# Performance work log

Hardware: AMD Instinct MI355X
Metric: run time of the kernel (lower is better)

## Reference

```python
import jax, jax.numpy as jnp
import numpy as np

EPS = 1e-9
NUM_HEADS = 16
D = 1024      # input_dim == hidden_dim
B, S = 2, 2048


def layer_norm(x, scale, shift):
    mu = x.mean(axis=-1, keepdims=True)
    # torch std is unbiased (ddof=1); eps added to std, not variance
    std = jnp.std(x, axis=-1, ddof=1, keepdims=True)
    return scale * (x - mu) / (std + EPS) + shift


def setup_inputs() -> dict:
    key = jax.random.key(0)
    ks = jax.random.split(key, 18)
    d, h = D, D
    w = lambda k, sh: jax.random.normal(k, sh, dtype=jnp.float32) * 0.02
    return {
        "inputs": jax.random.normal(ks[0], (B, S, d), dtype=jnp.float32),
        "ln1_scale": jax.random.normal(ks[1], (d,), dtype=jnp.float32),
        "ln1_shift": jax.random.normal(ks[2], (d,), dtype=jnp.float32),
        "Wq": w(ks[3], (d, h)), "bq": jnp.zeros((h,), jnp.float32),
        "Wk": w(ks[4], (d, h)), "bk": jnp.zeros((h,), jnp.float32),
        "Wv": w(ks[5], (d, h)), "bv": jnp.zeros((h,), jnp.float32),
        "Wo": w(ks[6], (h, d)), "bo": jnp.zeros((d,), jnp.float32),
        "W1": w(ks[7], (d, 4 * d)), "b1": jnp.zeros((4 * d,), jnp.float32),
        "W2": w(ks[8], (4 * d, d)), "b2": jnp.zeros((d,), jnp.float32),
        "ln2_scale": jax.random.normal(ks[9], (d,), dtype=jnp.float32),
        "ln2_shift": jax.random.normal(ks[10], (d,), dtype=jnp.float32),
    }


def mhsa(x, Wq, bq, Wk, bk, Wv, bv, Wo, bo):
    b, s, d = x.shape
    nh, dh = NUM_HEADS, D // NUM_HEADS
    q = (x @ Wq + bq).reshape(b, s, nh, dh).transpose(0, 2, 1, 3)  # b h s d
    k = (x @ Wk + bk).reshape(b, s, nh, dh).transpose(0, 2, 1, 3)
    v = (x @ Wv + bv).reshape(b, s, nh, dh).transpose(0, 2, 1, 3)
    scores = jnp.einsum("bhqd,bhkd->bhqk", q, k) / jnp.sqrt(jnp.float32(dh))
    causal = jnp.triu(jnp.ones((s, s), dtype=bool), k=1)  # mask above diagonal
    scores = jnp.where(causal, -jnp.inf, scores)
    p = jax.nn.softmax(scores, axis=-1)
    p = jnp.where(jnp.isnan(p), 0.0, p)  # NaN-fill as in original
    out = jnp.einsum("bhqk,bhkd->bhqd", p, v)
    out = out.transpose(0, 2, 1, 3).reshape(b, s, nh * dh)
    return out @ Wo + bo


def reference(inputs, ln1_scale, ln1_shift, Wq, bq, Wk, bk, Wv, bv, Wo, bo,
              W1, b1, W2, b2, ln2_scale, ln2_shift):
    o1 = layer_norm(inputs, ln1_scale, ln1_shift)
    o1 = mhsa(o1, Wq, bq, Wk, bk, Wv, bv, Wo, bo) + inputs
    o2 = layer_norm(o1, ln2_scale, ln2_shift)
    # NOTE: original adds the residual from the *normalized* tensor, not o1
    ffn = jax.nn.relu(o2 @ W1 + b1) @ W2 + b2
    return ffn + o2
```

## Files before the change

kernel.cpp:

```cpp
#include <hip/hip_runtime.h>
#include <hip/hip_bf16.h>
#include <math.h>

#define BB 2
#define SS 2048
#define DD 1024
#define HH 16
#define DH 64
#define NROW (BB*SS)
#define FFN (4*DD)

typedef __attribute__((ext_vector_type(8))) __bf16 bf16x8;
typedef __attribute__((ext_vector_type(4))) __bf16 bf16x4;
typedef __attribute__((ext_vector_type(4))) float f32x4;

#define QSCALE 0.18033688011112042f

__device__ __forceinline__ ushort f2b(float f) {
    union { float f; uint32_t u; } x; x.f = f;
    uint32_t r = x.u + 0x7FFF + ((x.u >> 16) & 1);
    return (ushort)(r >> 16);
}
__device__ __forceinline__ float b2f(ushort u) {
    union { uint32_t u; float f; } x; x.u = (uint32_t)u << 16;
    return x.f;
}

__global__ __launch_bounds__(256)
void ln_kernel(const float* __restrict__ x, const float* __restrict__ scale,
               const float* __restrict__ shift, ushort* __restrict__ y) {
    int row = blockIdx.x;
    const float* xr = x + (size_t)row * DD;
    ushort* yr = y + (size_t)row * DD;
    int t = threadIdx.x;
    float v[4];
    float s = 0.f, ss = 0.f;
#pragma unroll
    for (int i = 0; i < 4; ++i) {
        v[i] = xr[t + 256 * i];
        s += v[i];
        ss += v[i] * v[i];
    }
#pragma unroll
    for (int off = 32; off; off >>= 1) {
        s  += __shfl_xor(s, off);
        ss += __shfl_xor(ss, off);
    }
    __shared__ float red[8];
    int w = t >> 6;
    if ((t & 63) == 0) { red[w] = s; red[w + 4] = ss; }
    __syncthreads();
    float st  = red[0] + red[1] + red[2] + red[3];
    float sst = red[4] + red[5] + red[6] + red[7];
    float mu = st * (1.f / DD);
    float var = (sst - DD * mu * mu) * (1.f / (DD - 1));
    var = fmaxf(var, 0.f);
    float inv = 1.f / (sqrtf(var) + 1e-9f);
#pragma unroll
    for (int i = 0; i < 4; ++i) {
        int c = t + 256 * i;
        yr[c] = f2b(scale[c] * (v[i] - mu) * inv + shift[c]);
    }
}

__global__ __launch_bounds__(256)
void ln_res4_kernel(const ushort* __restrict__ p, const float* __restrict__ pbias,
                    const float* __restrict__ xb,
                    const float* __restrict__ scale, const float* __restrict__ shift,
                    ushort* __restrict__ yb) {
    const size_t MN = (size_t)NROW * DD;
    int row = blockIdx.x;
    ushort* ybr = yb + (size_t)row * DD;
    int t = threadIdx.x;
    float v[4];
    float s = 0.f, ss = 0.f;
#pragma unroll
    for (int i = 0; i < 4; ++i) {
        int c = t + 256 * i;
        size_t idx = (size_t)row * DD + c;
        float sum = b2f(p[idx]) + b2f(p[MN + idx]) + b2f(p[2 * MN + idx])
                  + b2f(p[3 * MN + idx]) + pbias[c] + xb[idx];
        v[i] = sum;
        s += sum;
        ss += sum * sum;
    }
#pragma unroll
    for (int off = 32; off; off >>= 1) {
        s  += __shfl_xor(s, off);
        ss += __shfl_xor(ss, off);
    }
    __shared__ float red[8];
    int w = t >> 6;
    if ((t & 63) == 0) { red[w] = s; red[w + 4] = ss; }
    __syncthreads();
    float st  = red[0] + red[1] + red[2] + red[3];
    float sst = red[4] + red[5] + red[6] + red[7];
    float mu = st * (1.f / DD);
    float var = (sst - DD * mu * mu) * (1.f / (DD - 1));
    var = fmaxf(var, 0.f);
    float inv = 1.f / (sqrtf(var) + 1e-9f);
#pragma unroll
    for (int i = 0; i < 4; ++i) {
        int c = t + 256 * i;
        ybr[c] = f2b(scale[c] * (v[i] - mu) * inv + shift[c]);
    }
}

__global__ __launch_bounds__(256)
void transpose_bf16_kernel(const float* __restrict__ W, ushort* __restrict__ Wt,
                           int K, int N) {
    __shared__ ushort tile[32][33];
    int tx = threadIdx.x & 31;
    int ty = threadIdx.x >> 5;
    int n0 = blockIdx.x * 32;
    int k0 = blockIdx.y * 32;
#pragma unroll
    for (int i = 0; i < 32; i += 8)
        tile[ty + i][tx] = f2b(W[(size_t)(k0 + ty + i) * N + n0 + tx]);
    __syncthreads();
#pragma unroll
    for (int i = 0; i < 32; i += 8)
        Wt[(size_t)(n0 + ty + i) * K + k0 + tx] = tile[tx][ty + i];
}

__global__ __launch_bounds__(256)
void transpose4_bf16_kernel(const float* __restrict__ W0, const float* __restrict__ W1,
                            const float* __restrict__ W2, const float* __restrict__ W3,
                            ushort* __restrict__ Wt) {
    __shared__ ushort tile[32][33];
    int z = blockIdx.z;
    const float* W = z == 0 ? W0 : (z == 1 ? W1 : (z == 2 ? W2 : W3));
    ushort* dst = Wt + (size_t)z * DD * DD;
    int tx = threadIdx.x & 31;
    int ty = threadIdx.x >> 5;
    int n0 = blockIdx.x * 32;
    int k0 = blockIdx.y * 32;
#pragma unroll
    for (int i = 0; i < 32; i += 8)
        tile[ty + i][tx] = f2b(W[(size_t)(k0 + ty + i) * DD + n0 + tx]);
    __syncthreads();
#pragma unroll
    for (int i = 0; i < 32; i += 8)
        dst[(size_t)(n0 + ty + i) * DD + k0 + tx] = tile[tx][ty + i];
}

__global__ __launch_bounds__(256)
void reduce_ffn2_kernel(const ushort* __restrict__ p, const float* __restrict__ bias,
                        const ushort* __restrict__ res, float* __restrict__ out) {
    const size_t MN = (size_t)NROW * DD;
    int i = (blockIdx.x * 256 + threadIdx.x) * 4;
    ushort4 a = *reinterpret_cast<const ushort4*>(p + i);
    ushort4 b = *reinterpret_cast<const ushort4*>(p + MN + i);
    ushort4 c4 = *reinterpret_cast<const ushort4*>(p + 2 * MN + i);
    ushort4 d4 = *reinterpret_cast<const ushort4*>(p + 3 * MN + i);
    ushort4 r = *reinterpret_cast<const ushort4*>(res + i);
    int c = i & (DD - 1);
    float4 bs = *reinterpret_cast<const float4*>(bias + c);
    float4 o;
    o.x = b2f(a.x) + b2f(b.x) + b2f(c4.x) + b2f(d4.x) + bs.x + b2f(r.x);
    o.y = b2f(a.y) + b2f(b.y) + b2f(c4.y) + b2f(d4.y) + bs.y + b2f(r.y);
    o.z = b2f(a.z) + b2f(b.z) + b2f(c4.z) + b2f(d4.z) + bs.z + b2f(r.z);
    o.w = b2f(a.w) + b2f(b.w) + b2f(c4.w) + b2f(d4.w) + bs.w + b2f(r.w);
    *reinterpret_cast<float4*>(out + i) = o;
}

#define GBM 128
#define GBK 32

template <int MODE, bool BF16_OUT, int DEPTH, int BN>
__global__ __launch_bounds__(512)
void gemm_bf16_kernel(const ushort* __restrict__ A, const ushort* __restrict__ Wt,
                      const float* __restrict__ bias, const ushort* __restrict__ addsrc,
                      void* __restrict__ Cout, int M, int N, int K, int lda,
                      const float* __restrict__ bias2, const float* __restrict__ bias3,
                      void* __restrict__ out2, void* __restrict__ out3) {
    __shared__ ushort As[DEPTH][GBM * GBK];
    __shared__ ushort Bs[DEPTH][BN * GBK];
    constexpr int NF = BN / 64;

    int tid = threadIdx.x;
    int lane = tid & 63;
    int wid = tid >> 6;
    int wr = wid >> 2, wc = wid & 3;

    int gx = gridDim.x;
    int nwg = gx * gridDim.y;
    int orig = blockIdx.y * gx + blockIdx.x;
    int q8 = nwg >> 3;
    int swz = (orig & 7) * q8 + (orig >> 3);
    int bx = swz % gx, by = swz / gx;

    int brow = by * GBM;
    int bcol = bx * BN;
    size_t koff = (size_t)blockIdx.z * K;

    int lrow = lane & 15;
    int kgrp = lane >> 4;

    f32x4 acc[4][NF] = {};

    auto stage = [&](int buf, int k0) {
        {
            int row = tid >> 2;
            int gran = (tid & 3) ^ ((row >> 1) & 3);
            const char* ga = (const char*)A +
                ((size_t)(brow + row) * lda + koff + k0) * 2 + gran * 16;
            __builtin_amdgcn_global_load_lds(
                (const __attribute__((address_space(1))) uint32_t*)ga,
                (__attribute__((address_space(3))) uint32_t*)(&As[buf][0] + (wid * 16) * GBK),
                16, 0, 0);
        }
#pragma unroll
        for (int i = 0; i < BN / 128; ++i) {
            int idx = i * 512 + tid;
            int row = idx >> 2;
            int gran = (idx & 3) ^ ((row >> 1) & 3);
            const char* gb = (const char*)Wt +
                ((size_t)(bcol + row) * lda + koff + k0) * 2 + gran * 16;
            __builtin_amdgcn_global_load_lds(
                (const __attribute__((address_space(1))) uint32_t*)gb,
                (__attribute__((address_space(3))) uint32_t*)(&Bs[buf][0] + (i * 128 + wid * 16) * GBK),
                16, 0, 0);
        }
    };

    int nk = K / GBK;
    constexpr int PRE = DEPTH - 1;
#pragma unroll
    for (int s = 0; s < PRE; ++s)
        if (s < nk) stage(s, s * GBK);

    int cur = 0, stg = PRE;
    for (int t = 0; t < nk; ++t) {
        __builtin_amdgcn_sched_barrier(0);
        int rem = nk - 1 - t;
        if constexpr (DEPTH == 3 && BN == 128) {
            if (rem >= 1)      asm volatile("s_waitcnt vmcnt(2)" ::: "memory");
            else               asm volatile("s_waitcnt vmcnt(0)" ::: "memory");
        } else if constexpr (DEPTH == 3 && BN == 256) {
            if (rem >= 1)      asm volatile("s_waitcnt vmcnt(3)" ::: "memory");
            else               asm volatile("s_waitcnt vmcnt(0)" ::: "memory");
        } else {
            asm volatile("s_waitcnt vmcnt(0)" ::: "memory");
        }
        asm volatile("s_barrier" ::: "memory");
        if (t + PRE < nk) stage(stg, (t + PRE) * GBK);

        bf16x8 afrag[4], bfrag[NF];
#pragma unroll
        for (int mi = 0; mi < 4; ++mi) {
            int row = wr * 64 + mi * 16 + lrow;
            int gran = kgrp ^ ((row >> 1) & 3);
            afrag[mi] = *(const bf16x8*)((const char*)&As[cur][0] + row * 64 + gran * 16);
        }
#pragma unroll
        for (int ni = 0; ni < NF; ++ni) {
            int row = wc * (BN / 4) + ni * 16 + lrow;
            int gran = kgrp ^ ((row >> 1) & 3);
            bfrag[ni] = *(const bf16x8*)((const char*)&Bs[cur][0] + row * 64 + gran * 16);
        }
#pragma unroll
        for (int mi = 0; mi < 4; ++mi)
#pragma unroll
            for (int ni = 0; ni < NF; ++ni)
                acc[mi][ni] = __builtin_amdgcn_mfma_f32_16x16x32_bf16(
                    afrag[mi], bfrag[ni], acc[mi][ni], 0, 0, 0);

        cur = (cur == DEPTH - 1) ? 0 : cur + 1;
        stg = (stg == DEPTH - 1) ? 0 : stg + 1;
    }

    if (MODE == 3) {
        int which = bcol >> 10;
        const float* bs = which == 0 ? bias : (which == 1 ? bias2 : bias3);
#pragma unroll
        for (int ni = 0; ni < NF; ++ni) {
            int col = bcol + wc * (BN / 4) + ni * 16 + lrow;
            int lcol = col & 1023;
            float bsv = bs[lcol];
#pragma unroll
            for (int mi = 0; mi < 4; ++mi) {
                f32x4 a = acc[mi][ni];
#pragma unroll
                for (int j = 0; j < 4; ++j) {
                    int row = brow + wr * 64 + mi * 16 + kgrp * 4 + j;
                    float val = a[j] + bsv;
                    if (which == 2) {
                        size_t idx = (size_t)(row >> 11) * ((size_t)DD * SS)
                                   + (size_t)lcol * SS + (row & (SS - 1));
                        ((ushort*)out3)[idx] = f2b(val);
                    } else if (which == 0) {
                        ((ushort*)Cout)[(size_t)row * DD + lcol] = f2b(val * QSCALE);
                    } else {
                        ((ushort*)out2)[(size_t)row * DD + lcol] = f2b(val);
                    }
                }
            }
        }
        return;
    }

    if (MODE == 4) {
        ushort* dst = (ushort*)Cout + (size_t)blockIdx.z * ((size_t)M * N);
#pragma unroll
        for (int ni = 0; ni < NF; ++ni) {
            int col = bcol + wc * (BN / 4) + ni * 16 + lrow;
#pragma unroll
            for (int mi = 0; mi < 4; ++mi) {
                f32x4 a = acc[mi][ni];
#pragma unroll
                for (int j = 0; j < 4; ++j) {
                    int row = brow + wr * 64 + mi * 16 + kgrp * 4 + j;
                    dst[(size_t)row * N + col] = f2b(a[j]);
                }
            }
        }
        return;
    }

#pragma unroll
    for (int ni = 0; ni < NF; ++ni) {
        int col = bcol + wc * (BN / 4) + ni * 16 + lrow;
        float bsv = bias[col];
#pragma unroll
        for (int mi = 0; mi < 4; ++mi) {
            f32x4 a = acc[mi][ni];
#pragma unroll
            for (int j = 0; j < 4; ++j) {
                int row = brow + wr * 64 + mi * 16 + kgrp * 4 + j;
                float val = a[j] + bsv;
                if (MODE == 1) val = fmaxf(val, 0.f);
                if (BF16_OUT)
                    ((ushort*)Cout)[(size_t)row * N + col] = f2b(val);
                else
                    ((float*)Cout)[(size_t)row * N + col] = val;
            }
        }
    }
}

__global__ __launch_bounds__(512)
void attn_mfma_kernel(const ushort* __restrict__ Qg, const ushort* __restrict__ Kg,
                      const ushort* __restrict__ Vtg, ushort* __restrict__ Og) {
    __shared__ ushort Qs[128 * 64];
    __shared__ ushort Ks[2][64 * 64];
    __shared__ ushort Vs[2][64 * 64];

    int tid = threadIdx.x;
    int lane = tid & 63;
    int wid = tid >> 6;
    int bh = blockIdx.x;
    int b = bh >> 4, h = bh & 15;
    int y = blockIdx.y;
    int pr = (y < 8) ? y : 23 - y;
    int qp0 = pr * 128;
    int nt = (qp0 >> 6) + 2;

    const ushort* Qbase = Qg + ((size_t)(b * SS + qp0)) * DD + h * DH;
    const ushort* Kbase = Kg + ((size_t)(b * SS)) * DD + h * DH;
    const ushort* Vbase = Vtg + (size_t)bh * DH * SS;

    int g = lane >> 4;
    int lr = lane & 15;

    auto stageKV = [&](int buf, int k0) {
        int rr = wid * 8 + (lane >> 3);
        int gg = (lane & 7) ^ (rr & 7);
        const ushort* srck = Kbase + (size_t)(k0 + rr) * DD + gg * 8;
        __builtin_amdgcn_global_load_lds(
            (const __attribute__((address_space(1))) uint32_t*)srck,
            (__attribute__((address_space(3))) uint32_t*)(&Ks[buf][0] + (wid * 8) * 64),
            16, 0, 0);
        const ushort* srcv = Vbase + (size_t)rr * SS + k0 + gg * 8;
        __builtin_amdgcn_global_load_lds(
            (const __attribute__((address_space(1))) uint32_t*)srcv,
            (__attribute__((address_space(3))) uint32_t*)(&Vs[buf][0] + (wid * 8) * 64),
            16, 0, 0);
    };

    {
        int rr0 = wid * 16 + (lane >> 3);
        int g0 = lane & 7;
#pragma unroll
        for (int i = 0; i < 2; ++i) {
            int rr = rr0 + i * 8;
            int gg = g0 ^ (rr & 7);
            const ushort* src = Qbase + (size_t)rr * DD + gg * 8;
            __builtin_amdgcn_global_load_lds(
                (const __attribute__((address_space(1))) uint32_t*)src,
                (__attribute__((address_space(3))) uint32_t*)(Qs + (wid * 16 + i * 8) * 64),
                16, 0, 0);
        }
    }
    stageKV(0, 0);
    asm volatile("s_waitcnt vmcnt(2)" ::: "memory");

    int offF[8];
#pragma unroll
    for (int ni = 0; ni < 4; ++ni)
#pragma unroll
        for (int ks = 0; ks < 2; ++ks) {
            int r = ni * 16 + lr;
            offF[ni * 2 + ks] = r * 128 + (((ks * 4 + g) ^ (r & 7)) << 4);
        }
    int rq = wid * 16 + lr;
    int offQ[2];
#pragma unroll
    for (int ks = 0; ks < 2; ++ks)
        offQ[ks] = rq * 128 + (((ks * 4 + g) ^ (rq & 7)) << 4);
    int offPw[4];
#pragma unroll
    for (int ni = 0; ni < 4; ++ni)
        offPw[ni] = rq * 128 + (((ni * 2 + (g >> 1)) ^ (rq & 7)) << 4) + (g & 1) * 8;

    bf16x8 aq[2];
#pragma unroll
    for (int ks = 0; ks < 2; ++ks)
        aq[ks] = *(const bf16x8*)((const char*)Qs + offQ[ks]);
    ushort* Ps = Qs;

    f32x4 oacc[4] = {};
    float m = -INFINITY, l = 0.f;
    const float THR = 11.0f;
    int qa = qp0 + wid * 16 + lr;
    int qw0 = qp0 + wid * 16;

    int cur = 0;
    for (int t = 0; t < nt; ++t) {
        __builtin_amdgcn_sched_barrier(0);
        asm volatile("s_waitcnt vmcnt(0)" ::: "memory");
        asm volatile("s_barrier" ::: "memory");
        if (t + 1 < nt) stageKV(cur ^ 1, (t + 1) * 64);
        int k0 = t * 64;

        f32x4 sacc[4] = {};
        __builtin_amdgcn_s_setprio(1);
#pragma unroll
        for (int ni = 0; ni < 4; ++ni)
#pragma unroll
            for (int ks = 0; ks < 2; ++ks) {
                bf16x8 bk = *(const bf16x8*)((const char*)&Ks[cur][0] + offF[ni * 2 + ks]);
                sacc[ni] = __builtin_amdgcn_mfma_f32_16x16x32_bf16(bk, aq[ks], sacc[ni], 0, 0, 0);
            }
        __builtin_amdgcn_s_setprio(0);

        if (k0 + 63 > qw0) {
#pragma unroll
            for (int ni = 0; ni < 4; ++ni) {
#pragma unroll
                for (int j = 0; j < 4; ++j) {
                    int key = k0 + ni * 16 + g * 4 + j;
                    if (key > qa) sacc[ni][j] = -INFINITY;
                }
            }
        }

        float mx = sacc[0][0];
#pragma unroll
        for (int ni = 0; ni < 4; ++ni)
#pragma unroll
            for (int j = 0; j < 4; ++j) mx = fmaxf(mx, sacc[ni][j]);
        mx = fmaxf(mx, __shfl_xor(mx, 16));
        mx = fmaxf(mx, __shfl_xor(mx, 32));

        if (__any(mx > m + THR)) {
            float mn = fmaxf(m, mx);
            float corr = __builtin_amdgcn_exp2f(m - mn);
            m = mn;
            l *= corr;
            float cj[4];
#pragma unroll
            for (int j = 0; j < 4; ++j)
                cj[j] = __shfl(corr, (lane & 48) | (g * 4 + j));
#pragma unroll
            for (int ni = 0; ni < 4; ++ni)
#pragma unroll
                for (int j = 0; j < 4; ++j) oacc[ni][j] *= cj[j];
        }

        float p[4][4];
        float rs = 0.f;
#pragma unroll
        for (int ni = 0; ni < 4; ++ni)
#pragma unroll
            for (int j = 0; j < 4; ++j) {
                p[ni][j] = __builtin_amdgcn_exp2f(sacc[ni][j] - m);
                rs += p[ni][j];
            }
        rs += __shfl_xor(rs, 16);
        rs += __shfl_xor(rs, 32);
        l += rs;

#pragma unroll
        for (int ni = 0; ni < 4; ++ni) {
            bf16x4 w4 = { (__bf16)p[ni][0], (__bf16)p[ni][1],
                          (__bf16)p[ni][2], (__bf16)p[ni][3] };
            *(bf16x4*)((char*)Ps + offPw[ni]) = w4;
        }
        asm volatile("s_waitcnt lgkmcnt(0)" ::: "memory");

        bf16x8 ap[2];
#pragma unroll
        for (int ks = 0; ks < 2; ++ks)
            ap[ks] = *(const bf16x8*)((const char*)Ps + offQ[ks]);
        __builtin_amdgcn_s_setprio(1);
#pragma unroll
        for (int ni = 0; ni < 4; ++ni)
#pragma unroll
            for (int ks = 0; ks < 2; ++ks) {
                bf16x8 bv = *(const bf16x8*)((const char*)&Vs[cur][0] + offF[ni * 2 + ks]);
                oacc[ni] = __builtin_amdgcn_mfma_f32_16x16x32_bf16(ap[ks], bv, oacc[ni], 0, 0, 0);
            }
        __builtin_amdgcn_s_setprio(0);
        cur ^= 1;
    }

#pragma unroll
    for (int j = 0; j < 4; ++j) {
        float lj = __shfl(l, (lane & 48) | (g * 4 + j));
        float inv = 1.f / lj;
        int gr = qp0 + wid * 16 + g * 4 + j;
#pragma unroll
        for (int ni = 0; ni < 4; ++ni) {
            int d = ni * 16 + lr;
            Og[((size_t)(b * SS + gr)) * DD + h * DH + d] = f2b(oacc[ni][j] * inv);
        }
    }
}

extern "C" void kernel_launch(void* const* d_in, const int* in_sizes, int n_in,
                              void* d_out, int out_size, void* d_ws, size_t ws_size,
                              hipStream_t stream) {
    const float* inputs    = (const float*)d_in[0];
    const float* ln1_scale = (const float*)d_in[1];
    const float* ln1_shift = (const float*)d_in[2];
    const float* Wq = (const float*)d_in[3];
    const float* bq = (const float*)d_in[4];
    const float* Wk = (const float*)d_in[5];
    const float* bk = (const float*)d_in[6];
    const float* Wv = (const float*)d_in[7];
    const float* bv = (const float*)d_in[8];
    const float* Wo = (const float*)d_in[9];
    const float* bo = (const float*)d_in[10];
    const float* W1 = (const float*)d_in[11];
    const float* b1 = (const float*)d_in[12];
    const float* W2 = (const float*)d_in[13];
    const float* b2 = (const float*)d_in[14];
    const float* ln2_scale = (const float*)d_in[15];
    const float* ln2_shift = (const float*)d_in[16];
    float* out = (float*)d_out;

    const size_t MB = 1024 * 1024;
    char* w = (char*)d_ws;
    ushort* q_b   = (ushort*)(w + 0 * MB);
    ushort* k_b   = (ushort*)(w + 8 * MB);
    ushort* vt_b  = (ushort*)(w + 16 * MB);
    ushort* att_b = (ushort*)(w + 24 * MB);
    ushort* pw    = (ushort*)(w + 32 * MB);
    ushort* o2_b  = (ushort*)(w + 8 * MB);
    ushort* pf    = (ushort*)(w + 16 * MB);
    ushort* h1_b  = (ushort*)(w + 64 * MB);
    ushort* wq_t  = (ushort*)(w + 96 * MB);
    ushort* wk_t  = (ushort*)(w + 98 * MB);
    ushort* wv_t  = (ushort*)(w + 100 * MB);
    ushort* wo_t  = (ushort*)(w + 102 * MB);
    ushort* w1_t  = (ushort*)(w + 104 * MB);
    ushort* w2_t  = (ushort*)(w + 112 * MB);
    ushort* xn_b  = (ushort*)(w + 120 * MB);

    transpose4_bf16_kernel<<<dim3(DD / 32, DD / 32, 4), 256, 0, stream>>>(
        Wq, Wk, Wv, Wo, wq_t);
    transpose_bf16_kernel<<<dim3(FFN / 32, DD / 32), 256, 0, stream>>>(W1, w1_t, DD, FFN);
    transpose_bf16_kernel<<<dim3(DD / 32, FFN / 32), 256, 0, stream>>>(W2, w2_t, FFN, DD);

    ln_kernel<<<NROW, 256, 0, stream>>>(inputs, ln1_scale, ln1_shift, xn_b);

    dim3 gqkv(3 * DD / 128, NROW / GBM, 1);
    gemm_bf16_kernel<3, true, 3, 128><<<gqkv, 512, 0, stream>>>(
        xn_b, wq_t, bq, nullptr, q_b, NROW, 3 * DD, DD, DD, bk, bv, k_b, vt_b);

    dim3 ga(BB * HH, SS / 128);
    attn_mfma_kernel<<<ga, 512, 0, stream>>>(q_b, k_b, vt_b, att_b);

    dim3 gwo(DD / 256, NROW / GBM, 4);
    gemm_bf16_kernel<4, false, 3, 256><<<gwo, 512, 0, stream>>>(
        att_b, wo_t, nullptr, nullptr, pw, NROW, DD, DD / 4, DD, nullptr, nullptr, nullptr, nullptr);

    ln_res4_kernel<<<NROW, 256, 0, stream>>>(pw, bo, inputs, ln2_scale, ln2_shift, o2_b);

    dim3 g2(FFN / 256, NROW / GBM, 1);
    gemm_bf16_kernel<1, true, 3, 256><<<g2, 512, 0, stream>>>(
        o2_b, w1_t, b1, nullptr, h1_b, NROW, FFN, DD, DD, nullptr, nullptr, nullptr, nullptr);

    dim3 gf2(DD / 256, NROW / GBM, 4);
    gemm_bf16_kernel<4, false, 3, 256><<<gf2, 512, 0, stream>>>(
        h1_b, w2_t, nullptr, nullptr, pf, NROW, DD, FFN / 4, FFN, nullptr, nullptr, nullptr, nullptr);
    reduce_ffn2_kernel<<<(NROW * DD / 4) / 256, 256, 0, stream>>>(pf, b2, o2_b, out);
}
```

Baseline: 228.4 us.

## Split causal attention KV range into two halves with separate combine kernel

Each attention query block's causal KV range is split across two blocks along a new grid z dimension. Each block writes an unnormalized bf16 partial output and per-row (max, sum) stats, and a new combine kernel merges them with log-sum-exp weights. This replaces the earlier paired-row load balancing with equal-length work per block and doubles the number of blocks. In exchange it adds extra global traffic for the partials, an extra kernel launch, and an extra bf16 rounding of the partial outputs.

```diff
diff --git a/kernel.cpp b/kernel.cpp
--- a/kernel.cpp
+++ b/kernel.cpp
@@ -15,6 +15,7 @@
 typedef __attribute__((ext_vector_type(4))) float f32x4;
 
 #define QSCALE 0.18033688011112042f
+#define NEG_BIG (-3.0e38f)
 
 __device__ __forceinline__ ushort f2b(float f) {
     union { float f; uint32_t u; } x; x.f = f;
@@ -164,6 +165,33 @@
     *reinterpret_cast<float4*>(out + i) = o;
 }
 
+__global__ __launch_bounds__(256)
+void attn_combine_kernel(const ushort* __restrict__ po, const float2* __restrict__ ml,
+                         ushort* __restrict__ att) {
+    const size_t MN = (size_t)NROW * DD;
+    int i = blockIdx.x * 256 + threadIdx.x;
+    int e = i * 4;
+    int d0 = e & (DD - 1);
+    int s = (e >> 10) & (SS - 1);
+    int b = e >> 21;
+    int h = d0 >> 6;
+    int bh = b * HH + h;
+    float2 ml0 = ml[(size_t)bh * SS + s];
+    float2 ml1 = ml[(size_t)(BB * HH) * SS + (size_t)bh * SS + s];
+    float M = fmaxf(ml0.x, ml1.x);
+    float w0 = __builtin_amdgcn_exp2f(ml0.x - M);
+    float w1 = __builtin_amdgcn_exp2f(ml1.x - M);
+    float inv = 1.f / (ml0.y * w0 + ml1.y * w1);
+    ushort4 a = *reinterpret_cast<const ushort4*>(po + e);
+    ushort4 c = *reinterpret_cast<const ushort4*>(po + MN + e);
+    ushort4 o;
+    o.x = f2b((b2f(a.x) * w0 + b2f(c.x) * w1) * inv);
+    o.y = f2b((b2f(a.y) * w0 + b2f(c.y) * w1) * inv);
+    o.z = f2b((b2f(a.z) * w0 + b2f(c.z) * w1) * inv);
+    o.w = f2b((b2f(a.w) * w0 + b2f(c.w) * w1) * inv);
+    *reinterpret_cast<ushort4*>(att + e) = o;
+}
+
 #define GBM 128
 #define GBK 32
 
@@ -341,7 +369,8 @@
 
 __global__ __launch_bounds__(512)
 void attn_mfma_kernel(const ushort* __restrict__ Qg, const ushort* __restrict__ Kg,
-                      const ushort* __restrict__ Vtg, ushort* __restrict__ Og) {
+                      const ushort* __restrict__ Vtg, ushort* __restrict__ Po,
+                      float2* __restrict__ Ml) {
     __shared__ ushort Qs[128 * 64];
     __shared__ ushort Ks[2][64 * 64];
     __shared__ ushort Vs[2][64 * 64];
@@ -351,10 +380,11 @@
     int wid = tid >> 6;
     int bh = blockIdx.x;
     int b = bh >> 4, h = bh & 15;
-    int y = blockIdx.y;
-    int pr = (y < 8) ? y : 23 - y;
+    int pr = blockIdx.y;
+    int z = blockIdx.z;
     int qp0 = pr * 128;
-    int nt = (qp0 >> 6) + 2;
+    int half = pr + 1;
+    int t0 = z * half;
 
     const ushort* Qbase = Qg + ((size_t)(b * SS + qp0)) * DD + h * DH;
     const ushort* Kbase = Kg + ((size_t)(b * SS)) * DD + h * DH;
@@ -392,7 +422,7 @@
                 16, 0, 0);
         }
     }
-    stageKV(0, 0);
+    stageKV(0, t0 * 64);
     asm volatile("s_waitcnt vmcnt(2)" ::: "memory");
 
     int offF[8];
@@ -420,17 +450,18 @@
     ushort* Ps = Qs;
 
     f32x4 oacc[4] = {};
-    float m = -INFINITY, l = 0.f;
+    float m = NEG_BIG, l = 0.f;
     const float THR = 11.0f;
     int qa = qp0 + wid * 16 + lr;
     int qw0 = qp0 + wid * 16;
 
     int cur = 0;
-    for (int t = 0; t < nt; ++t) {
+    for (int tt = 0; tt < half; ++tt) {
+        int t = t0 + tt;
         __builtin_amdgcn_sched_barrier(0);
         asm volatile("s_waitcnt vmcnt(0)" ::: "memory");
         asm volatile("s_barrier" ::: "memory");
-        if (t + 1 < nt) stageKV(cur ^ 1, (t + 1) * 64);
+        if (tt + 1 < half) stageKV(cur ^ 1, (t + 1) * 64);
         int k0 = t * 64;
 
         f32x4 sacc[4] = {};
@@ -515,16 +546,21 @@
         cur ^= 1;
     }
 
-#pragma unroll
-    for (int j = 0; j < 4; ++j) {
-        float lj = __shfl(l, (lane & 48) | (g * 4 + j));
-        float inv = 1.f / lj;
-        int gr = qp0 + wid * 16 + g * 4 + j;
-#pragma unroll
-        for (int ni = 0; ni < 4; ++ni) {
-            int d = ni * 16 + lr;
-            Og[((size_t)(b * SS + gr)) * DD + h * DH + d] = f2b(oacc[ni][j] * inv);
-        }
+    {
+        const size_t MN = (size_t)NROW * DD;
+        ushort* po = Po + (size_t)z * MN;
+#pragma unroll
+        for (int j = 0; j < 4; ++j) {
+            int gr = qp0 + wid * 16 + g * 4 + j;
+#pragma unroll
+            for (int ni = 0; ni < 4; ++ni) {
+                int d = ni * 16 + lr;
+                po[((size_t)(b * SS + gr)) * DD + h * DH + d] = f2b(oacc[ni][j]);
+            }
+        }
+        if (g == 0)
+            Ml[(size_t)z * ((size_t)BB * HH * SS) + (size_t)bh * SS + qa] =
+                make_float2(m, l);
     }
 }
 
@@ -556,6 +592,8 @@
     ushort* k_b   = (ushort*)(w + 8 * MB);
     ushort* vt_b  = (ushort*)(w + 16 * MB);
     ushort* att_b = (ushort*)(w + 24 * MB);
+    ushort* po_b  = (ushort*)(w + 32 * MB);
+    float2* ml_b  = (float2*)(w + 48 * MB);
     ushort* pw    = (ushort*)(w + 32 * MB);
     ushort* o2_b  = (ushort*)(w + 8 * MB);
     ushort* pf    = (ushort*)(w + 16 * MB);
@@ -579,8 +617,9 @@
     gemm_bf16_kernel<3, true, 3, 128><<<gqkv, 512, 0, stream>>>(
         xn_b, wq_t, bq, nullptr, q_b, NROW, 3 * DD, DD, DD, bk, bv, k_b, vt_b);
 
-    dim3 ga(BB * HH, SS / 128);
-    attn_mfma_kernel<<<ga, 512, 0, stream>>>(q_b, k_b, vt_b, att_b);
+    dim3 ga(BB * HH, SS / 128, 2);
+    attn_mfma_kernel<<<ga, 512, 0, stream>>>(q_b, k_b, vt_b, po_b, ml_b);
+    attn_combine_kernel<<<(NROW * DD / 4) / 256, 256, 0, stream>>>(po_b, ml_b, att_b);
 
     dim3 gwo(DD / 256, NROW / GBM, 4);
     gemm_bf16_kernel<4, false, 3, 256><<<gwo, 512, 0, stream>>>(
```

Result: no change. 231.3 us (+1.3%).
